# Optimization experiments

Hardware: AMD Instinct MI355X
Metric: run time of the kernel (lower is better)

The kernel has to match this reference:

```python
import jax, jax.numpy as jnp
import numpy as np

B, N, H = 32, 256, 1024
HEADS, NHID = 8, 128
NCLS = 7
BAND = 24
ALPHA = 0.2          # GAT leaky-relu slope
NEG = -9e15          # masked-attention fill, as in pyGAT


def setup_inputs() -> dict:
    key = jax.random.key(0)
    ks = jax.random.split(key, 16)
    def nrm(k, shp, s=0.02):
        return jax.random.normal(k, shp, dtype=jnp.float32) * s
    hidden_cls = jax.random.normal(ks[0], (B, N, H), dtype=jnp.float32)
    hidden_emo = jax.random.normal(ks[1], (B, N, H), dtype=jnp.float32)
    # causal band cliques, diagonal included (GAT uses clique - eye)
    t = jnp.arange(N)
    band = ((t[None, :] <= t[:, None]) & (t[None, :] > t[:, None] - BAND)).astype(jnp.float32)
    clique = jnp.broadcast_to(band, (B, N, N))
    labels = jax.random.randint(ks[2], (B, N), 0, NCLS)
    pooler_W = nrm(ks[3], (H, H)); pooler_b = jnp.zeros((H,), jnp.float32)
    gat_W = nrm(ks[4], (HEADS, H, NHID))
    gat_a1 = nrm(ks[5], (HEADS, NHID)); gat_a2 = nrm(ks[6], (HEADS, NHID))
    out_W = nrm(ks[7], (H, H))            # heads*nhid == H -> nclass=H
    out_a1 = nrm(ks[8], (H,)); out_a2 = nrm(ks[9], (H,))
    lin1_W = nrm(ks[10], (H, H)); lin1_b = jnp.zeros((H,), jnp.float32)
    lin0_W = nrm(ks[11], (2 * H, H)); lin0_b = jnp.zeros((H,), jnp.float32)
    cls_W = nrm(ks[12], (H, NCLS)); cls_b = jnp.zeros((NCLS,), jnp.float32)
    A = jax.random.uniform(ks[13], (NCLS, NCLS), dtype=jnp.float32) + 0.1
    hmm_A = A / A.sum(axis=1, keepdims=True)   # row-stochastic transition matrix
    return dict(hidden_cls=hidden_cls, hidden_emo=hidden_emo, clique=clique,
                labels=labels, pooler_W=pooler_W, pooler_b=pooler_b,
                gat_W=gat_W, gat_a1=gat_a1, gat_a2=gat_a2,
                out_W=out_W, out_a1=out_a1, out_a2=out_a2,
                lin1_W=lin1_W, lin1_b=lin1_b, lin0_W=lin0_W, lin0_b=lin0_b,
                cls_W=cls_W, cls_b=cls_b, hmm_A=hmm_A)


def _lrelu(x):
    return jnp.where(x > 0, x, ALPHA * x)


def reference(hidden_cls, hidden_emo, clique, labels, pooler_W, pooler_b,
              gat_W, gat_a1, gat_a2, out_W, out_a1, out_a2,
              lin1_W, lin1_b, lin0_W, lin0_b, cls_W, cls_b, hmm_A):
    # PoolerAll: dense + tanh on all token states (dropout = identity in eval)
    fea_cls = jnp.tanh(hidden_cls @ pooler_W + pooler_b)   # [B,N,H] (CLS per utt)
    fea_emo = jnp.tanh(hidden_emo @ pooler_W + pooler_b)   # [B,N,H] (mask tok per utt)

    eyeN = jnp.eye(N, dtype=clique.dtype)
    adjm = (clique - eyeN) > 0                             # [B,N,N] GAT adjacency

    def gat_one(x, am):                                    # x [N,H], am [N,N]
        Wh = jnp.einsum('nf,hfd->hnd', x, gat_W)           # [heads,N,nhid]
        e = _lrelu(jnp.einsum('hnd,hd->hn', Wh, gat_a1)[:, :, None]
                   + jnp.einsum('hnd,hd->hn', Wh, gat_a2)[:, None, :])
        att = jax.nn.softmax(jnp.where(am[None], e, NEG), axis=-1)
        h1 = jax.nn.elu(jnp.einsum('hnm,hmd->hnd', att, Wh))
        h1 = jnp.transpose(h1, (1, 0, 2)).reshape(N, HEADS * NHID)
        Wh2 = h1 @ out_W                                   # out attention layer (concat=False)
        e2 = _lrelu((Wh2 @ out_a1)[:, None] + (Wh2 @ out_a2)[None, :])
        h2 = jax.nn.softmax(jnp.where(am, e2, NEG), axis=-1) @ Wh2
        return jax.nn.elu(h2)                              # [N,H]

    gat_out = jax.vmap(gat_one)(fea_cls, adjm)             # [B,N,H]
    # row 0 replaced by (dropout of) fea_cls row 0, as in the original
    g = jnp.concatenate([fea_cls[:, :1], gat_out[:, 1:]], axis=1)
    g = jnp.concatenate([fea_cls, g @ lin1_W + lin1_b], axis=-1) @ lin0_W + lin0_b
    log_gat = jax.nn.softmax(g @ cls_W + cls_b, axis=-1)   # [B,N,NCLS] (probs)

    # HMM emission probs hmm_B(fea) = softmax(classifier(fea))
    Bprob = jax.nn.softmax(fea_emo @ cls_W + cls_b, axis=-1)  # [B,N,NCLS]
    P0 = jnp.full((NCLS,), 1.0 / NCLS, dtype=jnp.float32)
    AT = hmm_A.T

    def hmm_row(Bp, mrow):                                 # Bp [N,NCLS], mrow [N]
        def step(carry, xs):
            p, started = carry
            bt, m = xs
            p_init = P0 * bt; p_init = p_init / p_init.sum()
            p_tr = (AT @ p) * bt; p_tr = p_tr / p_tr.sum()
            p_new = jnp.where(started, p_tr, p_init)
            valid = m > 0.5
            return (jnp.where(valid, p_new, p), started | valid), None
        (p, _), _ = jax.lax.scan(step, (P0, jnp.asarray(False)), (Bp, mrow))
        return p                                           # final filtered posterior

    log_hmm = jax.vmap(lambda Bp, M: jax.vmap(lambda mr: hmm_row(Bp, mr))(M))(Bprob, clique)

    logits = jnp.log((log_gat + log_hmm) * 0.5).reshape(B * N, NCLS)
    lab = labels.reshape(B * N)
    mask = lab >= 0
    picked = jnp.take_along_axis(logits, jnp.where(mask, lab, 0)[:, None], axis=1)[:, 0]
    loss = -(jnp.where(mask, picked, 0.0).sum() / jnp.maximum(mask.sum(), 1).astype(jnp.float32))
    return loss, logits
```

## Files before the change

kernel.cpp:

```cpp
#include <hip/hip_runtime.h>
#include <hip/hip_bf16.h>
#include <math.h>

typedef __hip_bfloat16 bf16;
typedef __attribute__((ext_vector_type(8))) short short8;
typedef __attribute__((ext_vector_type(4))) float float4v;

static constexpr int Bb = 32, Nn = 256, Hh = 1024, HEADS = 8, NHID = 128, NCLS = 7, BAND = 24;
static constexpr int M = Bb * Nn;
static constexpr float ALPHA = 0.2f;
static constexpr long INEL = (long)M * Hh;

__device__ __forceinline__ float tof(bf16 x) { return __bfloat162float(x); }
__device__ __forceinline__ bf16 tob(float x) { return __float2bfloat16(x); }
__device__ __forceinline__ unsigned short f2bits(float x) {
    bf16 h = __float2bfloat16(x);
    return *(unsigned short*)&h;
}
__device__ __forceinline__ float bits2f(unsigned short u) {
    unsigned v = ((unsigned)u) << 16;
    float f;
    __builtin_memcpy(&f, &v, 4);
    return f;
}

__device__ __forceinline__ void gload16(const void* g, void* l) {
    __builtin_amdgcn_global_load_lds(
        (const __attribute__((address_space(1))) void*)g,
        (__attribute__((address_space(3))) void*)l, 16, 0, 0);
}

static constexpr long OFF_PWT  = 0;
static constexpr long OFF_PB   = 1048576;
static constexpr long OFF_WCT  = 1049600;
static constexpr long OFF_GA1  = 2098176;
static constexpr long OFF_GA2  = 2099200;
static constexpr long OFF_OWT  = 2100224;
static constexpr long OFF_OA1  = 3148800;
static constexpr long OFF_OA2  = 3149824;
static constexpr long OFF_CWT  = 6298624;
static constexpr long OFF_CB   = 6305792;
static constexpr long OFF_HA   = 6305799;
static constexpr long W_TOTAL  = 6305848;

__device__ __forceinline__ float ldany(const void* p, long i, int isb) {
    return isb ? tof(((const bf16*)p)[i]) : ((const float*)p)[i];
}

__device__ __forceinline__ int probe_dev(const void* pW, int t, int* sb) {
    int bad = 0;
    for (int i = t; i < 4096; i += 256) {
        float v = tof(((const bf16*)pW)[i]);
        if (!(fabsf(v) < 1e4f)) bad = 1;
    }
    sb[t] = bad; __syncthreads();
    for (int s = 128; s; s >>= 1) { if (t < s) sb[t] |= sb[t + s]; __syncthreads(); }
    int isb = sb[0] ? 0 : 1;
    __syncthreads();
    return isb;
}

__global__ __launch_bounds__(256) void prep1_k(
    const void* pW, const void* pb, const void* gW, const void* ga1,
    const void* ga2, const void* oW, const void* oa1, const void* oa2,
    const void* l0W, const void* cW, const void* cb, const void* hA,
    const void* in_emo, const void* in_cls,
    bf16* __restrict__ wc, int* __restrict__ flag,
    float* __restrict__ W1T, float* __restrict__ Gb,
    bf16* __restrict__ d0, bf16* __restrict__ d1) {
    __shared__ float SM[7168];
    const int bx = blockIdx.x;
    const int t = threadIdx.x;
    const int isb = probe_dev(pW, t, (int*)SM);

    if (bx == 0) {
        if (t == 0) *flag = isb;
        for (int i = t; i < 1024; i += 256) {
            wc[OFF_PB  + i] = tob(ldany(pb,  i, isb));
            wc[OFF_GA1 + i] = tob(ldany(ga1, i, isb));
            wc[OFF_GA2 + i] = tob(ldany(ga2, i, isb));
            wc[OFF_OA1 + i] = tob(ldany(oa1, i, isb));
            wc[OFF_OA2 + i] = tob(ldany(oa2, i, isb));
        }
        for (int i = t; i < 7168; i += 256) {
            int c = i >> 10, k = i & 1023;
            wc[OFF_CWT + i] = tob(ldany(cW, (long)k * 7 + c, isb));
        }
        if (t < NCLS) wc[OFF_CB + t] = tob(ldany(cb, t, isb));
        if (t < NCLS * NCLS) wc[OFF_HA + t] = tob(ldany(hA, t, isb));
        return;
    }
    if (bx < 1 + 2560) {
        int bi = bx - 1;
        int z = bi >> 8, rem = bi & 255;
        int bxx = rem & 15, byy = rem >> 4;
        float (*S)[65] = (float(*)[65])SM;
        const int tx = t & 63, ty0 = t >> 6;
        if (z < 2) {
            const void* src = z ? oW : pW;
            const long doff = z ? OFF_OWT : OFF_PWT;
            const int r0 = byy * 64, c0 = bxx * 64;
            #pragma unroll 4
            for (int it = 0; it < 16; ++it) {
                int ty = it * 4 + ty0;
                S[ty][tx] = ldany(src, (long)(r0 + ty) * 1024 + c0 + tx, isb);
            }
            __syncthreads();
            #pragma unroll 4
            for (int it = 0; it < 16; ++it) {
                int ty = it * 4 + ty0;
                wc[doff + (long)(c0 + ty) * 1024 + r0 + tx] = tob(S[tx][ty]);
            }
        } else {
            if (bxx >= 2) return;
            const int h = z - 2;
            const int r0 = byy * 64, c0 = bxx * 64;
            const long sbase = (long)h * 131072;
            #pragma unroll 4
            for (int it = 0; it < 16; ++it) {
                int ty = it * 4 + ty0;
                S[ty][tx] = ldany(gW, sbase + (long)(r0 + ty) * 128 + c0 + tx, isb);
            }
            __syncthreads();
            #pragma unroll 4
            for (int it = 0; it < 16; ++it) {
                int ty = it * 4 + ty0;
                wc[OFF_WCT + (long)(h * 128 + c0 + ty) * 1024 + r0 + tx] = tob(S[tx][ty]);
            }
        }
        return;
    }
    if (bx < 1 + 2560 + 256) {
        int bi = bx - 2561;
        float (*S)[NCLS] = (float(*)[NCLS])SM;
        for (int j = t; j < 1024; j += 256) {
            #pragma unroll
            for (int c = 0; c < NCLS; ++c) S[j][c] = ldany(cW, (long)j * 7 + c, isb);
        }
        __syncthreads();
        const int wave = t >> 6, lane = t & 63;
        #pragma unroll
        for (int r = 0; r < 2; ++r) {
            int k = bi * 8 + wave * 2 + r;
            float acc[NCLS];
            #pragma unroll
            for (int c = 0; c < NCLS; ++c) acc[c] = 0.f;
            #pragma unroll
            for (int q = 0; q < 16; ++q) {
                int j = lane * 16 + q;
                float x = ldany(l0W, (long)k * 1024 + j, isb);
                #pragma unroll
                for (int c = 0; c < NCLS; ++c) acc[c] += x * S[j][c];
            }
            #pragma unroll
            for (int c = 0; c < NCLS; ++c)
                #pragma unroll
                for (int off = 32; off; off >>= 1) acc[c] += __shfl_down(acc[c], off);
            if (lane == 0) {
                #pragma unroll
                for (int c = 0; c < NCLS; ++c) {
                    if (k < 1024) W1T[c * 1024 + k] = acc[c];
                    else          Gb[(k - 1024) * 7 + c] = acc[c];
                }
            }
        }
        return;
    }
    if (isb) return;
    long bi = bx - 2817;
    long i = (bi * 256 + t) * 8;
    const void* s; bf16* d; long off;
    if (i < INEL) { s = in_emo; d = d0; off = i; }
    else          { s = in_cls; d = d1; off = i - INEL; }
    const float* f = (const float*)s + off;
    unsigned short tmp[8];
    #pragma unroll
    for (int q = 0; q < 8; ++q) tmp[q] = f2bits(f[q]);
    *(int4*)(d + off) = *(int4*)tmp;
}

__global__ __launch_bounds__(256) void prep2_k(const int* __restrict__ flagp,
                                               const void* __restrict__ l1W,
                                               const void* __restrict__ l1b,
                                               const void* __restrict__ l0b,
                                               const void* __restrict__ cW,
                                               const void* __restrict__ cb,
                                               const float* __restrict__ Gb,
                                               float* __restrict__ W2T,
                                               float* __restrict__ cvec) {
    __shared__ float S[1024][NCLS];
    const int bx = blockIdx.x;
    const int t = threadIdx.x;
    const int isb = *flagp;
    if (bx < 128) {
        for (int j = t; j < 1024; j += 256) {
            #pragma unroll
            for (int c = 0; c < NCLS; ++c) S[j][c] = Gb[(long)j * 7 + c];
        }
        __syncthreads();
        const int wave = t >> 6, lane = t & 63;
        #pragma unroll
        for (int r = 0; r < 2; ++r) {
            int i = bx * 8 + wave * 2 + r;
            float acc[NCLS];
            #pragma unroll
            for (int c = 0; c < NCLS; ++c) acc[c] = 0.f;
            #pragma unroll
            for (int q = 0; q < 16; ++q) {
                int o = lane * 16 + q;
                float x = ldany(l1W, (long)i * 1024 + o, isb);
                #pragma unroll
                for (int c = 0; c < NCLS; ++c) acc[c] += x * S[o][c];
            }
            #pragma unroll
            for (int c = 0; c < NCLS; ++c)
                #pragma unroll
                for (int off = 32; off; off >>= 1) acc[c] += __shfl_down(acc[c], off);
            if (lane == 0) {
                #pragma unroll
                for (int c = 0; c < NCLS; ++c) W2T[c * 1024 + i] = acc[c];
            }
        }
        return;
    }
    if (t >= 64) return;
    int lane = t;
    float acc[NCLS];
    #pragma unroll
    for (int c = 0; c < NCLS; ++c) acc[c] = 0.f;
    for (int o = lane; o < 1024; o += 64) {
        float b1 = ldany(l1b, o, isb);
        float b0 = ldany(l0b, o, isb);
        #pragma unroll
        for (int c = 0; c < NCLS; ++c)
            acc[c] += b1 * Gb[o * 7 + c] + b0 * ldany(cW, (long)o * 7 + c, isb);
    }
    #pragma unroll
    for (int c = 0; c < NCLS; ++c)
        #pragma unroll
        for (int off = 32; off; off >>= 1) acc[c] += __shfl_down(acc[c], off);
    if (lane == 0) {
        #pragma unroll
        for (int c = 0; c < NCLS; ++c) cvec[c] = acc[c] + ldany(cb, c, isb);
    }
}

static constexpr int SLOT_US = 256 * 32;

template <int ACT, int DOTS>
__device__ __forceinline__ void gemm_pipe_core(
    const bf16* __restrict__ A, int strideA,
    const bf16* __restrict__ Bt, int strideB,
    const bf16* __restrict__ bias, bf16* __restrict__ Cout,
    int Nc, int K, int bm, int bn, unsigned short* lds,
    const bf16* __restrict__ oa1 = nullptr, const bf16* __restrict__ oa2 = nullptr,
    float* __restrict__ f1b = nullptr, float* __restrict__ f2b = nullptr) {
    const int tid = threadIdx.x;
    const int lane = tid & 63;
    const int wave = tid >> 6;
    const int wm = (wave >> 1) * 64, wn = (wave & 1) * 64;
    const int l15 = lane & 15, quad = lane >> 4;
    const int csw = ((lane & 3) ^ ((lane >> 2) & 3) ^ (lane >> 4)) * 8;
    const int sc8 = (quad ^ (l15 & 3) ^ (l15 >> 2)) * 8;

    long aoff[2], boff[2];
    #pragma unroll
    for (int o = 0; o < 2; ++o) {
        aoff[o] = (long)(bm + wave * 32 + o * 16 + (lane >> 2)) * strideA + csw;
        boff[o] = (long)(bn + wave * 32 + o * 16 + (lane >> 2)) * strideB + csw;
    }
    const int aDst = wave * 32 * 32;
    const int bDst = (128 + wave * 32) * 32;

    const int nt = K / 32;
    float4v acc[4][4];
    #pragma unroll
    for (int i = 0; i < 4; ++i)
        #pragma unroll
        for (int j = 0; j < 4; ++j) acc[i][j] = (float4v){0.f, 0.f, 0.f, 0.f};

    auto stage = [&](int ts, int slot) {
        unsigned short* buf = lds + slot * SLOT_US;
        int k = ts * 32;
        gload16(A + aoff[0] + k, buf + aDst);
        gload16(A + aoff[1] + k, buf + aDst + 512);
        gload16(Bt + boff[0] + k, buf + bDst);
        gload16(Bt + boff[1] + k, buf + bDst + 512);
    };
    auto frags = [&](int slot, short8* af, short8* bfr) {
        const unsigned short* bufc = lds + slot * SLOT_US;
        #pragma unroll
        for (int i = 0; i < 4; ++i)
            af[i] = *(const short8*)(bufc + (wm + i * 16 + l15) * 32 + sc8);
        #pragma unroll
        for (int j = 0; j < 4; ++j)
            bfr[j] = *(const short8*)(bufc + (128 + wn + j * 16 + l15) * 32 + sc8);
    };

    stage(0, 0); stage(1, 1); stage(2, 2);
    asm volatile("s_waitcnt vmcnt(8)" ::: "memory");
    __builtin_amdgcn_s_barrier();
    asm volatile("" ::: "memory");
    short8 afA[4], bfA[4], afB[4], bfB[4];
    frags(0, afA, bfA);
    int c0 = 0, c1 = 1, c2 = 2;

    for (int t = 0; t < nt; t += 2) {
        asm volatile("s_waitcnt lgkmcnt(0)" ::: "memory");
        if (t < nt - 2) asm volatile("s_waitcnt vmcnt(4)" ::: "memory");
        else            asm volatile("s_waitcnt vmcnt(0)" ::: "memory");
        __builtin_amdgcn_s_barrier();
        asm volatile("" ::: "memory");
        if (t + 3 < nt) stage(t + 3, c0);
        if (t + 1 < nt) frags(c1, afB, bfB);
        __builtin_amdgcn_s_setprio(1);
        #pragma unroll
        for (int i = 0; i < 4; ++i)
            #pragma unroll
            for (int j = 0; j < 4; ++j)
                acc[i][j] = __builtin_amdgcn_mfma_f32_16x16x32_bf16(afA[i], bfA[j], acc[i][j], 0, 0, 0);
        __builtin_amdgcn_s_setprio(0);
        asm volatile("" ::: "memory");
        asm volatile("s_waitcnt lgkmcnt(0)" ::: "memory");
        if (t + 1 < nt - 2) asm volatile("s_waitcnt vmcnt(4)" ::: "memory");
        else                asm volatile("s_waitcnt vmcnt(0)" ::: "memory");
        __builtin_amdgcn_s_barrier();
        asm volatile("" ::: "memory");
        if (t + 4 < nt) stage(t + 4, c1);
        if (t + 2 < nt) frags(c2, afA, bfA);
        __builtin_amdgcn_s_setprio(1);
        #pragma unroll
        for (int i = 0; i < 4; ++i)
            #pragma unroll
            for (int j = 0; j < 4; ++j)
                acc[i][j] = __builtin_amdgcn_mfma_f32_16x16x32_bf16(afB[i], bfB[j], acc[i][j], 0, 0, 0);
        __builtin_amdgcn_s_setprio(0);
        asm volatile("" ::: "memory");
        int n0 = c2, n1 = c0, n2 = c1;
        c0 = n0; c1 = n1; c2 = n2;
    }

    #pragma unroll
    for (int j = 0; j < 4; ++j) {
        int gn = bn + wn + j * 16 + l15;
        float bj = bias ? tof(bias[gn]) : 0.f;
        #pragma unroll
        for (int i = 0; i < 4; ++i) {
            #pragma unroll
            for (int r = 0; r < 4; ++r) {
                int gm = bm + wm + i * 16 + quad * 4 + r;
                float v = acc[i][j][r] + bj;
                if (ACT == 1) v = tanhf(v);
                Cout[(long)gm * Nc + gn] = tob(v);
            }
        }
    }
    if (DOTS) {
        float o1v[4], o2v[4];
        #pragma unroll
        for (int j = 0; j < 4; ++j) {
            int gn = bn + wn + j * 16 + l15;
            o1v[j] = tof(oa1[gn]); o2v[j] = tof(oa2[gn]);
        }
        #pragma unroll
        for (int i = 0; i < 4; ++i) {
            #pragma unroll
            for (int r = 0; r < 4; ++r) {
                int gm = bm + wm + i * 16 + quad * 4 + r;
                float p1 = 0.f, p2 = 0.f;
                #pragma unroll
                for (int j = 0; j < 4; ++j) {
                    float v = bits2f(f2bits(acc[i][j][r]));
                    p1 += v * o1v[j]; p2 += v * o2v[j];
                }
                #pragma unroll
                for (int m = 1; m < 16; m <<= 1) {
                    p1 += __shfl_xor(p1, m); p2 += __shfl_xor(p2, m);
                }
                if (l15 == 0) { atomicAdd(&f1b[gm], p1); atomicAdd(&f2b[gm], p2); }
            }
        }
    }
}

__global__ __launch_bounds__(256, 3) void gemmP_pipe_k(const int* __restrict__ flagp,
                                                       const bf16* __restrict__ rawE,
                                                       const bf16* __restrict__ rawC,
                                                       const bf16* __restrict__ A0,
                                                       const bf16* __restrict__ A1,
                                                       const bf16* __restrict__ Bt,
                                                       const bf16* __restrict__ bias,
                                                       bf16* __restrict__ C0,
                                                       bf16* __restrict__ C1) {
    __shared__ __align__(16) unsigned short lds[3 * SLOT_US];
    const int isb = *flagp;
    const bf16* A = blockIdx.z ? (isb ? rawC : A1) : (isb ? rawE : A0);
    bf16* C = blockIdx.z ? C1 : C0;
    gemm_pipe_core<1, 0>(A, Hh, Bt, Hh, bias, C, Hh, Hh,
                         blockIdx.x * 128, blockIdx.y * 128, lds);
}

__global__ __launch_bounds__(256, 3) void gemm_cls_k(const bf16* __restrict__ A,
                                                     const bf16* __restrict__ Bt,
                                                     bf16* __restrict__ Cout,
                                                     const bf16* __restrict__ X,
                                                     const bf16* __restrict__ Wt,
                                                     const bf16* __restrict__ cb,
                                                     float* __restrict__ Bout) {
    __shared__ __align__(16) unsigned short lds[3 * SLOT_US];
    const int bx = blockIdx.x;
    if (bx < 512) {
        gemm_pipe_core<0, 0>(A, Hh, Bt, Hh, (const bf16*)nullptr, Cout, Hh, Hh,
                             (bx & 63) * 128, (bx >> 6) * 128, lds);
        return;
    }
    const int t = threadIdx.x, wave = t >> 6, lane = t & 63;
    const int row = (bx - 512) * 4 + wave;
    float xv[16];
    {
        const bf16* x = X + (long)row * Hh + lane * 16;
        union { int4 v; unsigned short us[8]; } u0, u1;
        u0.v = *(const int4*)x; u1.v = *(const int4*)(x + 8);
        #pragma unroll
        for (int q = 0; q < 8; ++q) { xv[q] = bits2f(u0.us[q]); xv[q + 8] = bits2f(u1.us[q]); }
    }
    float acc[NCLS];
    #pragma unroll
    for (int cc = 0; cc < NCLS; ++cc) {
        const bf16* wr = Wt + (long)cc * Hh + lane * 16;
        union { int4 v; unsigned short us[8]; } w0, w1;
        w0.v = *(const int4*)wr; w1.v = *(const int4*)(wr + 8);
        float s = 0.f;
        #pragma unroll
        for (int q = 0; q < 8; ++q) {
            s += xv[q] * bits2f(w0.us[q]);
            s += xv[q + 8] * bits2f(w1.us[q]);
        }
        acc[cc] = s;
    }
    #pragma unroll
    for (int cc = 0; cc < NCLS; ++cc)
        #pragma unroll
        for (int off = 32; off; off >>= 1) acc[cc] += __shfl_down(acc[cc], off);
    if (lane == 0) {
        float mx = -1e30f;
        #pragma unroll
        for (int cc = 0; cc < NCLS; ++cc) { acc[cc] += tof(cb[cc]); mx = fmaxf(mx, acc[cc]); }
        float s = 0.f;
        #pragma unroll
        for (int cc = 0; cc < NCLS; ++cc) { acc[cc] = expf(acc[cc] - mx); s += acc[cc]; }
        float inv = 1.0f / s;
        #pragma unroll
        for (int cc = 0; cc < NCLS; ++cc) Bout[(long)row * NCLS + cc] = acc[cc] * inv;
    }
}

__global__ __launch_bounds__(256, 3) void gemm_f12_k(const bf16* __restrict__ A,
                                                     const bf16* __restrict__ Bt,
                                                     bf16* __restrict__ Cout,
                                                     const bf16* __restrict__ oa1,
                                                     const bf16* __restrict__ oa2,
                                                     float* __restrict__ f1b,
                                                     float* __restrict__ f2b) {
    __shared__ __align__(16) unsigned short lds[3 * SLOT_US];
    gemm_pipe_core<0, 1>(A, Hh, Bt, Hh, (const bf16*)nullptr, Cout, Hh, Hh,
                         blockIdx.x * 128, blockIdx.y * 128, lds, oa1, oa2, f1b, f2b);
}

__global__ __launch_bounds__(256) void att1f_k(const bf16* __restrict__ Wh,
                                               const bf16* __restrict__ ga1,
                                               const bf16* __restrict__ ga2,
                                               bf16* __restrict__ h1) {
    __shared__ unsigned short S[152][128];
    __shared__ float f1s[152], f2s[152];
    __shared__ float att[128][25];
    const int bx = blockIdx.x;
    const int t = threadIdx.x;
    const int wave = t >> 6, lane = t & 63;
    if (bx < 256) {
        int h = bx & 7, b = bx >> 3;
        float s0 = 0.f, s1 = 0.f;
        long base = (long)(b * 256) * 1024 + h * 128 + lane * 2;
        for (int m = wave * 64; m < wave * 64 + 64; ++m) {
            unsigned u = *(const unsigned*)(Wh + base + (long)m * 1024);
            s0 += bits2f((unsigned short)(u & 0xffff));
            s1 += bits2f((unsigned short)(u >> 16));
        }
        float* red = (float*)S;
        red[(wave * 64 + lane) * 2]     = s0;
        red[(wave * 64 + lane) * 2 + 1] = s1;
        __syncthreads();
        if (wave == 0) {
            s0 = red[lane * 2] + red[(64 + lane) * 2] + red[(128 + lane) * 2] + red[(192 + lane) * 2];
            s1 = red[lane * 2 + 1] + red[(64 + lane) * 2 + 1] + red[(128 + lane) * 2 + 1] + red[(192 + lane) * 2 + 1];
            s0 *= (1.0f / 256.0f); s1 *= (1.0f / 256.0f);
            s0 = s0 > 0.f ? s0 : expm1f(s0);
            s1 = s1 > 0.f ? s1 : expm1f(s1);
            unsigned out = (unsigned)f2bits(s0) | ((unsigned)f2bits(s1) << 16);
            *(unsigned*)(h1 + base) = out;
        }
        return;
    }
    const int bxm = bx - 256;
    const int b = bxm >> 4, h = (bxm >> 1) & 7, half = bxm & 1;
    const int nbase = half * 128;
    const int mstart = half ? (nbase - (BAND - 1)) : 0;
    const int mcount = half ? (256 - mstart) : 128;
    const int c = t & 15;

    float av1[8], av2[8];
    {
        union { int4 v; unsigned short us[8]; } u1, u2;
        u1.v = *(const int4*)(ga1 + h * 128 + c * 8);
        u2.v = *(const int4*)(ga2 + h * 128 + c * 8);
        #pragma unroll
        for (int qq = 0; qq < 8; ++qq) { av1[qq] = bits2f(u1.us[qq]); av2[qq] = bits2f(u2.us[qq]); }
    }

    const int iters = (mcount * 16 + 255) >> 8;
    for (int i = 0; i < iters; ++i) {
        int li = i * 256 + t;
        int mr = li >> 4;
        if (mr < mcount) {
            long ga = (long)(b * 256 + mstart + mr) * 1024 + h * 128 + c * 8;
            union { int4 v; unsigned short us[8]; } u;
            u.v = *(const int4*)(Wh + ga);
            float p1 = 0.f, p2 = 0.f;
            #pragma unroll
            for (int qq = 0; qq < 8; ++qq) {
                float f = bits2f(u.us[qq]);
                p1 += f * av1[qq]; p2 += f * av2[qq];
            }
            *(int4*)&S[mr][c * 8] = u.v;
            #pragma unroll
            for (int mask = 1; mask < 16; mask <<= 1) {
                p1 += __shfl_xor(p1, mask);
                p2 += __shfl_xor(p2, mask);
            }
            if (c == 0) { f1s[mr] = p1; f2s[mr] = p2; }
        }
    }
    __syncthreads();

    if (t < 128) {
        int n = nbase + t;
        if (n > 0) {
            int cnt = n < (BAND - 1) ? n : (BAND - 1);
            int m0 = n - cnt;
            float f1n = f1s[n - mstart];
            float e[BAND - 1];
            float mx = -1e30f;
            for (int i = 0; i < cnt; ++i) {
                float v = f1n + f2s[m0 + i - mstart];
                v = v > 0.f ? v : ALPHA * v;
                e[i] = v; mx = fmaxf(mx, v);
            }
            float ss = 0.f;
            for (int i = 0; i < cnt; ++i) { e[i] = __expf(e[i] - mx); ss += e[i]; }
            float inv = 1.0f / ss;
            for (int i = 0; i < cnt; ++i) att[t][i] = e[i] * inv;
        }
    }
    __syncthreads();

    for (int ln = wave; ln < 128; ln += 4) {
        int n = nbase + ln;
        if (n == 0) continue;
        int cnt = n < (BAND - 1) ? n : (BAND - 1);
        int mr0 = n - cnt - mstart;
        float s0 = 0.f, s1 = 0.f;
        for (int i = 0; i < cnt; ++i) {
            float a = att[ln][i];
            unsigned u = *(const unsigned*)&S[mr0 + i][lane * 2];
            s0 += a * bits2f((unsigned short)(u & 0xffff));
            s1 += a * bits2f((unsigned short)(u >> 16));
        }
        s0 = s0 > 0.f ? s0 : expm1f(s0);
        s1 = s1 > 0.f ? s1 : expm1f(s1);
        unsigned out = (unsigned)f2bits(s0) | ((unsigned)f2bits(s1) << 16);
        *(unsigned*)(h1 + (long)(b * 256 + n) * 1024 + h * 128 + lane * 2) = out;
    }
}

__global__ __launch_bounds__(256) void att2f_hmm_k(const bf16* __restrict__ Wh2,
                                                   const float* __restrict__ f1b,
                                                   const float* __restrict__ f2b,
                                                   bf16* __restrict__ g,
                                                   const float* __restrict__ Bprob,
                                                   const bf16* __restrict__ hmm_A,
                                                   float* __restrict__ lhmm) {
    __shared__ unsigned short S[152][128];
    __shared__ float att[128][25];
    __shared__ float AT[NCLS][NCLS];
    const int bx = blockIdx.x;
    const int t = threadIdx.x;
    if (bx >= 512) {
        if (t < NCLS * NCLS) {
            int i = t / NCLS, j = t % NCLS;
            AT[i][j] = tof(hmm_A[j * NCLS + i]);
        }
        __syncthreads();
        int idx = (bx - 512) * 256 + t;
        int n = idx & 255, b = idx >> 8;
        int t0 = n - (BAND - 1) > 0 ? n - (BAND - 1) : 0;
        const float* Bp = Bprob + (long)(b * 256) * NCLS;
        float p[NCLS];
        float s = 0.f;
        #pragma unroll
        for (int cc = 0; cc < NCLS; ++cc) { p[cc] = Bp[t0 * NCLS + cc]; s += p[cc]; }
        float inv = 1.0f / s;
        #pragma unroll
        for (int cc = 0; cc < NCLS; ++cc) p[cc] *= inv;
        for (int tt = t0 + 1; tt <= n; ++tt) {
            float q[NCLS]; float ss = 0.f;
            #pragma unroll
            for (int i = 0; i < NCLS; ++i) {
                float a = 0.f;
                #pragma unroll
                for (int j = 0; j < NCLS; ++j) a += AT[i][j] * p[j];
                a *= Bp[tt * NCLS + i];
                q[i] = a; ss += a;
            }
            float iv = 1.0f / ss;
            #pragma unroll
            for (int i = 0; i < NCLS; ++i) p[i] = q[i] * iv;
        }
        #pragma unroll
        for (int cc = 0; cc < NCLS; ++cc) lhmm[(long)idx * NCLS + cc] = p[cc];
        return;
    }
    const int b = bx >> 4, half = (bx >> 3) & 1, jt = bx & 7;
    const int nbase = half * 128;
    const int mstart = half ? (nbase - (BAND - 1)) : 0;
    const int mcount = half ? (256 - mstart) : 128;
    const int c = t & 15;

    const int iters = (mcount * 16 + 255) >> 8;
    for (int i = 0; i < iters; ++i) {
        int li = i * 256 + t;
        int mr = li >> 4;
        if (mr < mcount) {
            long ga = (long)(b * 256 + mstart + mr) * 1024 + jt * 128 + c * 8;
            *(int4*)&S[mr][c * 8] = *(const int4*)(Wh2 + ga);
        }
    }
    __syncthreads();

    if (t < 128) {
        int n = nbase + t;
        if (n > 0) {
            int cnt = n < (BAND - 1) ? n : (BAND - 1);
            int m0 = n - cnt;
            float f1n = f1b[b * 256 + n];
            float e[BAND - 1];
            float mx = -1e30f;
            for (int i = 0; i < cnt; ++i) {
                float v = f1n + f2b[b * 256 + m0 + i];
                v = v > 0.f ? v : ALPHA * v;
                e[i] = v; mx = fmaxf(mx, v);
            }
            float ss = 0.f;
            for (int i = 0; i < cnt; ++i) { e[i] = __expf(e[i] - mx); ss += e[i]; }
            float inv = 1.0f / ss;
            for (int i = 0; i < cnt; ++i) att[t][i] = e[i] * inv;
        }
    }
    __syncthreads();

    const int wave = t >> 6, lane = t & 63;
    for (int ln = wave; ln < 128; ln += 4) {
        int n = nbase + ln;
        if (n == 0) continue;
        int cnt = n < (BAND - 1) ? n : (BAND - 1);
        int mr0 = n - cnt - mstart;
        float s0 = 0.f, s1 = 0.f;
        for (int i = 0; i < cnt; ++i) {
            float a = att[ln][i];
            unsigned u = *(const unsigned*)&S[mr0 + i][lane * 2];
            s0 += a * bits2f((unsigned short)(u & 0xffff));
            s1 += a * bits2f((unsigned short)(u >> 16));
        }
        s0 = s0 > 0.f ? s0 : expm1f(s0);
        s1 = s1 > 0.f ? s1 : expm1f(s1);
        unsigned out = (unsigned)f2bits(s0) | ((unsigned)f2bits(s1) << 16);
        *(unsigned*)(g + (long)(b * 256 + n) * 1024 + jt * 128 + lane * 2) = out;
    }
}

__global__ __launch_bounds__(256) void lgf_k(const bf16* __restrict__ X,
                                             const bf16* __restrict__ Y,
                                             const float* __restrict__ W1T,
                                             const float* __restrict__ W2T,
                                             const float* __restrict__ cvec,
                                             const float* __restrict__ lhmm,
                                             const int* __restrict__ labels,
                                             void* __restrict__ out,
                                             float* __restrict__ blocksum,
                                             const int* __restrict__ flagp) {
    __shared__ float ps[4];
    const int t = threadIdx.x, wave = t >> 6, lane = t & 63;
    const int row = blockIdx.x * 4 + wave;
    const int isb = *flagp;
    const bf16* ybase = (row & 255) ? Y : X;
    float xv[16], yv[16];
    {
        const bf16* x = X + (long)row * 1024 + lane * 16;
        const bf16* y = ybase + (long)row * 1024 + lane * 16;
        union { int4 v; unsigned short us[8]; } u0, u1, v0, v1;
        u0.v = *(const int4*)x; u1.v = *(const int4*)(x + 8);
        v0.v = *(const int4*)y; v1.v = *(const int4*)(y + 8);
        #pragma unroll
        for (int q = 0; q < 8; ++q) {
            xv[q] = bits2f(u0.us[q]); xv[q + 8] = bits2f(u1.us[q]);
            yv[q] = bits2f(v0.us[q]); yv[q + 8] = bits2f(v1.us[q]);
        }
    }
    float acc[NCLS];
    #pragma unroll
    for (int cc = 0; cc < NCLS; ++cc) {
        const float4* w1 = (const float4*)(W1T + (long)cc * 1024 + lane * 16);
        const float4* w2 = (const float4*)(W2T + (long)cc * 1024 + lane * 16);
        float s = 0.f;
        #pragma unroll
        for (int h = 0; h < 4; ++h) {
            float4 a = w1[h], b = w2[h];
            s += xv[h * 4 + 0] * a.x + xv[h * 4 + 1] * a.y + xv[h * 4 + 2] * a.z + xv[h * 4 + 3] * a.w;
            s += yv[h * 4 + 0] * b.x + yv[h * 4 + 1] * b.y + yv[h * 4 + 2] * b.z + yv[h * 4 + 3] * b.w;
        }
        acc[cc] = s;
    }
    #pragma unroll
    for (int cc = 0; cc < NCLS; ++cc)
        #pragma unroll
        for (int off = 32; off; off >>= 1) acc[cc] += __shfl_down(acc[cc], off);
    if (lane == 0) {
        float mx = -1e30f;
        #pragma unroll
        for (int cc = 0; cc < NCLS; ++cc) { acc[cc] += cvec[cc]; mx = fmaxf(mx, acc[cc]); }
        float s = 0.f;
        #pragma unroll
        for (int cc = 0; cc < NCLS; ++cc) { acc[cc] = expf(acc[cc] - mx); s += acc[cc]; }
        float inv = 1.0f / s;
        int lab = labels[row];
        float picked = 0.f;
        #pragma unroll
        for (int cc = 0; cc < NCLS; ++cc) {
            float pg = acc[cc] * inv;
            float v = logf(0.5f * (pg + lhmm[(long)row * NCLS + cc]));
            long o = 1 + (long)row * NCLS + cc;
            if (isb) ((bf16*)out)[o] = tob(v);
            else     ((float*)out)[o] = v;
            if (cc == lab) picked = v;
        }
        ps[wave] = picked;
    }
    __syncthreads();
    if (t == 0) blocksum[blockIdx.x] = ps[0] + ps[1] + ps[2] + ps[3];
}

__global__ __launch_bounds__(256) void loss2_k(const float* __restrict__ blocksum,
                                               void* __restrict__ out,
                                               const int* __restrict__ flagp) {
    __shared__ float red[256];
    const int t = threadIdx.x;
    float s = 0.f;
    #pragma unroll
    for (int i = 0; i < 8; ++i) s += blocksum[t + i * 256];
    red[t] = s; __syncthreads();
    for (int st = 128; st; st >>= 1) {
        if (t < st) red[t] += red[t + st];
        __syncthreads();
    }
    if (t == 0) {
        float v = -red[0] / (float)(Bb * Nn);
        if (*flagp) ((bf16*)out)[0] = tob(v);
        else        ((float*)out)[0] = v;
    }
}

extern "C" void kernel_launch(void* const* d_in, const int* in_sizes, int n_in,
                              void* d_out, int out_size, void* d_ws, size_t ws_size,
                              hipStream_t stream) {
    const void* hidden_cls = d_in[0];
    const void* hidden_emo = d_in[1];
    const int* labels = (const int*)d_in[3];

    char* w = (char*)d_ws;
    bf16* C  = (bf16*)w;
    bf16* E  = C + INEL;
    bf16* Wb = E + INEL;
    bf16* H2 = Wb + INEL;
    bf16* wc = H2 + INEL;
    float* f1b      = (float*)(wc + W_TOTAL);
    float* f2b      = f1b + M;
    float* blocksum = f2b + M;
    int*   flag  = (int*)(blocksum + 2048);
    float* Bprob = (float*)(flag + 1);
    float* lhmm  = Bprob + (long)M * NCLS;
    float* W1f   = lhmm + (long)M * NCLS;
    float* W2f   = W1f + 7 * 1024;
    float* Gbf   = W2f + 7 * 1024;
    float* cvec  = Gbf + 1024 * 7;

    dim3 gblk(256);

    prep1_k<<<11009, gblk, 0, stream>>>(
        d_in[4], d_in[5], d_in[6], d_in[7], d_in[8], d_in[9], d_in[10], d_in[11],
        d_in[14], d_in[16], d_in[17], d_in[18], hidden_emo, hidden_cls,
        wc, flag, W1f, Gbf, Wb, H2);
    prep2_k<<<129, gblk, 0, stream>>>(flag, d_in[12], d_in[13], d_in[15],
                                      d_in[16], d_in[17], Gbf, W2f, cvec);
    gemmP_pipe_k<<<dim3(64, 8, 2), gblk, 0, stream>>>(
        flag, (const bf16*)hidden_emo, (const bf16*)hidden_cls, Wb, H2,
        wc + OFF_PWT, wc + OFF_PB, E, C);
    gemm_cls_k<<<512 + 2048, gblk, 0, stream>>>(C, wc + OFF_WCT, Wb,
                                                E, wc + OFF_CWT, wc + OFF_CB, Bprob);
    att1f_k<<<768, gblk, 0, stream>>>(Wb, wc + OFF_GA1, wc + OFF_GA2, E);
    (void)hipMemsetAsync(f1b, 0, (size_t)(2 * M) * 4, stream);
    gemm_f12_k<<<dim3(64, 8), gblk, 0, stream>>>(E, wc + OFF_OWT, Wb,
                                                 wc + OFF_OA1, wc + OFF_OA2, f1b, f2b);
    att2f_hmm_k<<<512 + 32, gblk, 0, stream>>>(Wb, f1b, f2b, E,
                                               Bprob, wc + OFF_HA, lhmm);
    lgf_k<<<2048, gblk, 0, stream>>>(C, E, W1f, W2f, cvec, lhmm, labels,
                                     d_out, blocksum, flag);
    loss2_k<<<1, gblk, 0, stream>>>(blocksum, d_out, flag);
}
```

Measured before the change: 461.7 us.

## Fuse all stages into one cooperative persistent kernel with grid syncs

Merges the prep, GEMM, attention, HMM and loss kernels into a single cooperative kernel. Blocks loop over the tasks of each phase, and grid-wide barriers separate the phases. This removes per-launch overhead and the separate memset, and the dtype probe now runs in every block instead of being passed through a flag. In exchange, the grid is capped at occupancy-limited size with a large shared-memory union, which may reduce GEMM occupancy and parallelism, and grid barriers add their own cost.

Result: slower. 888.4 us (+92.4%).

```diff
diff --git a/kernel.cpp b/kernel.cpp
--- a/kernel.cpp
+++ b/kernel.cpp
@@ -1,6 +1,9 @@
 #include <hip/hip_runtime.h>
 #include <hip/hip_bf16.h>
+#include <hip/hip_cooperative_groups.h>
 #include <math.h>
+
+namespace cg = cooperative_groups;
 
 typedef __hip_bfloat16 bf16;
 typedef __attribute__((ext_vector_type(8))) short short8;
@@ -43,9 +46,35 @@
 static constexpr long OFF_HA   = 6305799;
 static constexpr long W_TOTAL  = 6305848;
 
+static constexpr int SLOT_US = 256 * 32;
+
 __device__ __forceinline__ float ldany(const void* p, long i, int isb) {
     return isb ? tof(((const bf16*)p)[i]) : ((const float*)p)[i];
 }
+
+union ShU {
+    int sb[256];
+    unsigned short gemm[3 * SLOT_US];
+    float prep[7168];
+    struct { unsigned short S[152][128];
+             float f1s[152], f2s[152];
+             float att[128][25]; } a1;
+    struct { unsigned short S[152][128];
+             float att[128][25];
+             float AT[NCLS][NCLS]; } a2;
+    float ps[4];
+    float red[256];
+};
+
+struct MegaArgs {
+    const void *pW, *pb, *gW, *ga1, *ga2, *oW, *oa1, *oa2;
+    const void *l1W, *l1b, *l0W, *l0b, *cW, *cb, *hA;
+    const void *in_emo, *in_cls;
+    const int* labels;
+    bf16 *wc, *C, *E, *Wb, *H2;
+    float *f1b, *f2b, *blocksum, *Bprob, *lhmm, *W1T, *W2T, *Gb, *cvec;
+    void* out;
+};
 
 __device__ __forceinline__ int probe_dev(const void* pW, int t, int* sb) {
     int bad = 0;
@@ -60,44 +89,31 @@
     return isb;
 }
 
-__global__ __launch_bounds__(256) void prep1_k(
-    const void* pW, const void* pb, const void* gW, const void* ga1,
-    const void* ga2, const void* oW, const void* oa1, const void* oa2,
-    const void* l0W, const void* cW, const void* cb, const void* hA,
-    const void* in_emo, const void* in_cls,
-    bf16* __restrict__ wc, int* __restrict__ flag,
-    float* __restrict__ W1T, float* __restrict__ Gb,
-    bf16* __restrict__ d0, bf16* __restrict__ d1) {
-    __shared__ float SM[7168];
-    const int bx = blockIdx.x;
-    const int t = threadIdx.x;
-    const int isb = probe_dev(pW, t, (int*)SM);
-
-    if (bx == 0) {
-        if (t == 0) *flag = isb;
-        for (int i = t; i < 1024; i += 256) {
-            wc[OFF_PB  + i] = tob(ldany(pb,  i, isb));
-            wc[OFF_GA1 + i] = tob(ldany(ga1, i, isb));
-            wc[OFF_GA2 + i] = tob(ldany(ga2, i, isb));
-            wc[OFF_OA1 + i] = tob(ldany(oa1, i, isb));
-            wc[OFF_OA2 + i] = tob(ldany(oa2, i, isb));
-        }
-        for (int i = t; i < 7168; i += 256) {
-            int c = i >> 10, k = i & 1023;
-            wc[OFF_CWT + i] = tob(ldany(cW, (long)k * 7 + c, isb));
-        }
-        if (t < NCLS) wc[OFF_CB + t] = tob(ldany(cb, t, isb));
-        if (t < NCLS * NCLS) wc[OFF_HA + t] = tob(ldany(hA, t, isb));
-        return;
-    }
-    if (bx < 1 + 2560) {
-        int bi = bx - 1;
-        int z = bi >> 8, rem = bi & 255;
+__device__ void smalls_task(const MegaArgs& a, int t, int isb) {
+    bf16* wc = a.wc;
+    for (int i = t; i < 1024; i += 256) {
+        wc[OFF_PB  + i] = tob(ldany(a.pb,  i, isb));
+        wc[OFF_GA1 + i] = tob(ldany(a.ga1, i, isb));
+        wc[OFF_GA2 + i] = tob(ldany(a.ga2, i, isb));
+        wc[OFF_OA1 + i] = tob(ldany(a.oa1, i, isb));
+        wc[OFF_OA2 + i] = tob(ldany(a.oa2, i, isb));
+    }
+    for (int i = t; i < 7168; i += 256) {
+        int c = i >> 10, k = i & 1023;
+        wc[OFF_CWT + i] = tob(ldany(a.cW, (long)k * 7 + c, isb));
+    }
+    if (t < NCLS) wc[OFF_CB + t] = tob(ldany(a.cb, t, isb));
+    if (t < NCLS * NCLS) wc[OFF_HA + t] = tob(ldany(a.hA, t, isb));
+}
+
+__device__ void prep_mid_task(int v, const MegaArgs& a, int t, int isb, ShU* sh) {
+    if (v < 2560) {
+        int z = v >> 8, rem = v & 255;
         int bxx = rem & 15, byy = rem >> 4;
-        float (*S)[65] = (float(*)[65])SM;
+        float (*S)[65] = (float(*)[65])sh->prep;
         const int tx = t & 63, ty0 = t >> 6;
         if (z < 2) {
-            const void* src = z ? oW : pW;
+            const void* src = z ? a.oW : a.pW;
             const long doff = z ? OFF_OWT : OFF_PWT;
             const int r0 = byy * 64, c0 = bxx * 64;
             #pragma unroll 4
@@ -109,7 +125,7 @@
             #pragma unroll 4
             for (int it = 0; it < 16; ++it) {
                 int ty = it * 4 + ty0;
-                wc[doff + (long)(c0 + ty) * 1024 + r0 + tx] = tob(S[tx][ty]);
+                a.wc[doff + (long)(c0 + ty) * 1024 + r0 + tx] = tob(S[tx][ty]);
             }
         } else {
             if (bxx >= 2) return;
@@ -119,121 +135,96 @@
             #pragma unroll 4
             for (int it = 0; it < 16; ++it) {
                 int ty = it * 4 + ty0;
-                S[ty][tx] = ldany(gW, sbase + (long)(r0 + ty) * 128 + c0 + tx, isb);
+                S[ty][tx] = ldany(a.gW, sbase + (long)(r0 + ty) * 128 + c0 + tx, isb);
             }
             __syncthreads();
             #pragma unroll 4
             for (int it = 0; it < 16; ++it) {
                 int ty = it * 4 + ty0;
-                wc[OFF_WCT + (long)(h * 128 + c0 + ty) * 1024 + r0 + tx] = tob(S[tx][ty]);
+                a.wc[OFF_WCT + (long)(h * 128 + c0 + ty) * 1024 + r0 + tx] = tob(S[tx][ty]);
             }
         }
         return;
     }
-    if (bx < 1 + 2560 + 256) {
-        int bi = bx - 2561;
-        float (*S)[NCLS] = (float(*)[NCLS])SM;
-        for (int j = t; j < 1024; j += 256) {
-            #pragma unroll
-            for (int c = 0; c < NCLS; ++c) S[j][c] = ldany(cW, (long)j * 7 + c, isb);
-        }
-        __syncthreads();
-        const int wave = t >> 6, lane = t & 63;
-        #pragma unroll
-        for (int r = 0; r < 2; ++r) {
-            int k = bi * 8 + wave * 2 + r;
-            float acc[NCLS];
-            #pragma unroll
-            for (int c = 0; c < NCLS; ++c) acc[c] = 0.f;
-            #pragma unroll
-            for (int q = 0; q < 16; ++q) {
-                int j = lane * 16 + q;
-                float x = ldany(l0W, (long)k * 1024 + j, isb);
-                #pragma unroll
-                for (int c = 0; c < NCLS; ++c) acc[c] += x * S[j][c];
-            }
-            #pragma unroll
-            for (int c = 0; c < NCLS; ++c)
-                #pragma unroll
-                for (int off = 32; off; off >>= 1) acc[c] += __shfl_down(acc[c], off);
-            if (lane == 0) {
-                #pragma unroll
-                for (int c = 0; c < NCLS; ++c) {
-                    if (k < 1024) W1T[c * 1024 + k] = acc[c];
-                    else          Gb[(k - 1024) * 7 + c] = acc[c];
-                }
-            }
-        }
-        return;
-    }
-    if (isb) return;
-    long bi = bx - 2817;
-    long i = (bi * 256 + t) * 8;
-    const void* s; bf16* d; long off;
-    if (i < INEL) { s = in_emo; d = d0; off = i; }
-    else          { s = in_cls; d = d1; off = i - INEL; }
-    const float* f = (const float*)s + off;
-    unsigned short tmp[8];
-    #pragma unroll
-    for (int q = 0; q < 8; ++q) tmp[q] = f2bits(f[q]);
-    *(int4*)(d + off) = *(int4*)tmp;
-}
-
-__global__ __launch_bounds__(256) void prep2_k(const int* __restrict__ flagp,
-                                               const void* __restrict__ l1W,
-                                               const void* __restrict__ l1b,
-                                               const void* __restrict__ l0b,
-                                               const void* __restrict__ cW,
-                                               const void* __restrict__ cb,
-                                               const float* __restrict__ Gb,
-                                               float* __restrict__ W2T,
-                                               float* __restrict__ cvec) {
-    __shared__ float S[1024][NCLS];
-    const int bx = blockIdx.x;
-    const int t = threadIdx.x;
-    const int isb = *flagp;
-    if (bx < 128) {
-        for (int j = t; j < 1024; j += 256) {
-            #pragma unroll
-            for (int c = 0; c < NCLS; ++c) S[j][c] = Gb[(long)j * 7 + c];
-        }
-        __syncthreads();
-        const int wave = t >> 6, lane = t & 63;
-        #pragma unroll
-        for (int r = 0; r < 2; ++r) {
-            int i = bx * 8 + wave * 2 + r;
-            float acc[NCLS];
-            #pragma unroll
-            for (int c = 0; c < NCLS; ++c) acc[c] = 0.f;
-            #pragma unroll
-            for (int q = 0; q < 16; ++q) {
-                int o = lane * 16 + q;
-                float x = ldany(l1W, (long)i * 1024 + o, isb);
-                #pragma unroll
-                for (int c = 0; c < NCLS; ++c) acc[c] += x * S[o][c];
-            }
-            #pragma unroll
-            for (int c = 0; c < NCLS; ++c)
-                #pragma unroll
-                for (int off = 32; off; off >>= 1) acc[c] += __shfl_down(acc[c], off);
-            if (lane == 0) {
-                #pragma unroll
-                for (int c = 0; c < NCLS; ++c) W2T[c * 1024 + i] = acc[c];
-            }
-        }
-        return;
-    }
+    int bi = v - 2560;
+    float (*S)[NCLS] = (float(*)[NCLS])sh->prep;
+    for (int j = t; j < 1024; j += 256) {
+        #pragma unroll
+        for (int c = 0; c < NCLS; ++c) S[j][c] = ldany(a.cW, (long)j * 7 + c, isb);
+    }
+    __syncthreads();
+    const int wave = t >> 6, lane = t & 63;
+    #pragma unroll
+    for (int r = 0; r < 2; ++r) {
+        int k = bi * 8 + wave * 2 + r;
+        float acc[NCLS];
+        #pragma unroll
+        for (int c = 0; c < NCLS; ++c) acc[c] = 0.f;
+        #pragma unroll
+        for (int q = 0; q < 16; ++q) {
+            int j = lane * 16 + q;
+            float x = ldany(a.l0W, (long)k * 1024 + j, isb);
+            #pragma unroll
+            for (int c = 0; c < NCLS; ++c) acc[c] += x * S[j][c];
+        }
+        #pragma unroll
+        for (int c = 0; c < NCLS; ++c)
+            #pragma unroll
+            for (int off = 32; off; off >>= 1) acc[c] += __shfl_down(acc[c], off);
+        if (lane == 0) {
+            #pragma unroll
+            for (int c = 0; c < NCLS; ++c) {
+                if (k < 1024) a.W1T[c * 1024 + k] = acc[c];
+                else          a.Gb[(k - 1024) * 7 + c] = acc[c];
+            }
+        }
+    }
+}
+
+__device__ void w2_task(int bi, const MegaArgs& a, int t, int isb, ShU* sh) {
+    float (*S)[NCLS] = (float(*)[NCLS])sh->prep;
+    for (int j = t; j < 1024; j += 256) {
+        #pragma unroll
+        for (int c = 0; c < NCLS; ++c) S[j][c] = a.Gb[(long)j * 7 + c];
+    }
+    __syncthreads();
+    const int wave = t >> 6, lane = t & 63;
+    #pragma unroll
+    for (int r = 0; r < 2; ++r) {
+        int i = bi * 8 + wave * 2 + r;
+        float acc[NCLS];
+        #pragma unroll
+        for (int c = 0; c < NCLS; ++c) acc[c] = 0.f;
+        #pragma unroll
+        for (int q = 0; q < 16; ++q) {
+            int o = lane * 16 + q;
+            float x = ldany(a.l1W, (long)i * 1024 + o, isb);
+            #pragma unroll
+            for (int c = 0; c < NCLS; ++c) acc[c] += x * S[o][c];
+        }
+        #pragma unroll
+        for (int c = 0; c < NCLS; ++c)
+            #pragma unroll
+            for (int off = 32; off; off >>= 1) acc[c] += __shfl_down(acc[c], off);
+        if (lane == 0) {
+            #pragma unroll
+            for (int c = 0; c < NCLS; ++c) a.W2T[c * 1024 + i] = acc[c];
+        }
+    }
+}
+
+__device__ void cvec_task(const MegaArgs& a, int t, int isb) {
     if (t >= 64) return;
     int lane = t;
     float acc[NCLS];
     #pragma unroll
     for (int c = 0; c < NCLS; ++c) acc[c] = 0.f;
     for (int o = lane; o < 1024; o += 64) {
-        float b1 = ldany(l1b, o, isb);
-        float b0 = ldany(l0b, o, isb);
+        float b1 = ldany(a.l1b, o, isb);
+        float b0 = ldany(a.l0b, o, isb);
         #pragma unroll
         for (int c = 0; c < NCLS; ++c)
-            acc[c] += b1 * Gb[o * 7 + c] + b0 * ldany(cW, (long)o * 7 + c, isb);
+            acc[c] += b1 * a.Gb[o * 7 + c] + b0 * ldany(a.cW, (long)o * 7 + c, isb);
     }
     #pragma unroll
     for (int c = 0; c < NCLS; ++c)
@@ -241,11 +232,9 @@
         for (int off = 32; off; off >>= 1) acc[c] += __shfl_down(acc[c], off);
     if (lane == 0) {
         #pragma unroll
-        for (int c = 0; c < NCLS; ++c) cvec[c] = acc[c] + ldany(cb, c, isb);
-    }
-}
-
-static constexpr int SLOT_US = 256 * 32;
+        for (int c = 0; c < NCLS; ++c) a.cvec[c] = acc[c] + ldany(a.cb, c, isb);
+    }
+}
 
 template <int ACT, int DOTS>
 __device__ __forceinline__ void gemm_pipe_core(
@@ -383,39 +372,10 @@
     }
 }
 
-__global__ __launch_bounds__(256, 3) void gemmP_pipe_k(const int* __restrict__ flagp,
-                                                       const bf16* __restrict__ rawE,
-                                                       const bf16* __restrict__ rawC,
-                                                       const bf16* __restrict__ A0,
-                                                       const bf16* __restrict__ A1,
-                                                       const bf16* __restrict__ Bt,
-                                                       const bf16* __restrict__ bias,
-                                                       bf16* __restrict__ C0,
-                                                       bf16* __restrict__ C1) {
-    __shared__ __align__(16) unsigned short lds[3 * SLOT_US];
-    const int isb = *flagp;
-    const bf16* A = blockIdx.z ? (isb ? rawC : A1) : (isb ? rawE : A0);
-    bf16* C = blockIdx.z ? C1 : C0;
-    gemm_pipe_core<1, 0>(A, Hh, Bt, Hh, bias, C, Hh, Hh,
-                         blockIdx.x * 128, blockIdx.y * 128, lds);
-}
-
-__global__ __launch_bounds__(256, 3) void gemm_cls_k(const bf16* __restrict__ A,
-                                                     const bf16* __restrict__ Bt,
-                                                     bf16* __restrict__ Cout,
-                                                     const bf16* __restrict__ X,
-                                                     const bf16* __restrict__ Wt,
-                                                     const bf16* __restrict__ cb,
-                                                     float* __restrict__ Bout) {
-    __shared__ __align__(16) unsigned short lds[3 * SLOT_US];
-    const int bx = blockIdx.x;
-    if (bx < 512) {
-        gemm_pipe_core<0, 0>(A, Hh, Bt, Hh, (const bf16*)nullptr, Cout, Hh, Hh,
-                             (bx & 63) * 128, (bx >> 6) * 128, lds);
-        return;
-    }
-    const int t = threadIdx.x, wave = t >> 6, lane = t & 63;
-    const int row = (bx - 512) * 4 + wave;
+__device__ void cls7_task(int vt, const bf16* X, const bf16* Wt, const bf16* cb,
+                          float* Bout, int t) {
+    const int wave = t >> 6, lane = t & 63;
+    const int row = vt * 4 + wave;
     float xv[16];
     {
         const bf16* x = X + (long)row * Hh + lane * 16;
@@ -455,30 +415,11 @@
     }
 }
 
-__global__ __launch_bounds__(256, 3) void gemm_f12_k(const bf16* __restrict__ A,
-                                                     const bf16* __restrict__ Bt,
-                                                     bf16* __restrict__ Cout,
-                                                     const bf16* __restrict__ oa1,
-                                                     const bf16* __restrict__ oa2,
-                                                     float* __restrict__ f1b,
-                                                     float* __restrict__ f2b) {
-    __shared__ __align__(16) unsigned short lds[3 * SLOT_US];
-    gemm_pipe_core<0, 1>(A, Hh, Bt, Hh, (const bf16*)nullptr, Cout, Hh, Hh,
-                         blockIdx.x * 128, blockIdx.y * 128, lds, oa1, oa2, f1b, f2b);
-}
-
-__global__ __launch_bounds__(256) void att1f_k(const bf16* __restrict__ Wh,
-                                               const bf16* __restrict__ ga1,
-                                               const bf16* __restrict__ ga2,
-                                               bf16* __restrict__ h1) {
-    __shared__ unsigned short S[152][128];
-    __shared__ float f1s[152], f2s[152];
-    __shared__ float att[128][25];
-    const int bx = blockIdx.x;
-    const int t = threadIdx.x;
+__device__ void att1_task(int v, const bf16* Wh, const bf16* ga1, const bf16* ga2,
+                          bf16* h1, int t, ShU* sh) {
     const int wave = t >> 6, lane = t & 63;
-    if (bx < 256) {
-        int h = bx & 7, b = bx >> 3;
+    if (v < 256) {
+        int h = v & 7, b = v >> 3;
         float s0 = 0.f, s1 = 0.f;
         long base = (long)(b * 256) * 1024 + h * 128 + lane * 2;
         for (int m = wave * 64; m < wave * 64 + 64; ++m) {
@@ -486,7 +427,7 @@
             s0 += bits2f((unsigned short)(u & 0xffff));
             s1 += bits2f((unsigned short)(u >> 16));
         }
-        float* red = (float*)S;
+        float* red = (float*)sh;
         red[(wave * 64 + lane) * 2]     = s0;
         red[(wave * 64 + lane) * 2 + 1] = s1;
         __syncthreads();
@@ -501,7 +442,7 @@
         }
         return;
     }
-    const int bxm = bx - 256;
+    const int bxm = v - 256;
     const int b = bxm >> 4, h = (bxm >> 1) & 7, half = bxm & 1;
     const int nbase = half * 128;
     const int mstart = half ? (nbase - (BAND - 1)) : 0;
@@ -510,9 +451,9 @@
 
     float av1[8], av2[8];
     {
-        union { int4 v; unsigned short us[8]; } u1, u2;
-        u1.v = *(const int4*)(ga1 + h * 128 + c * 8);
-        u2.v = *(const int4*)(ga2 + h * 128 + c * 8);
+        union { int4 v4; unsigned short us[8]; } u1, u2;
+        u1.v4 = *(const int4*)(ga1 + h * 128 + c * 8);
+        u2.v4 = *(const int4*)(ga2 + h * 128 + c * 8);
         #pragma unroll
         for (int qq = 0; qq < 8; ++qq) { av1[qq] = bits2f(u1.us[qq]); av2[qq] = bits2f(u2.us[qq]); }
     }
@@ -523,21 +464,21 @@
         int mr = li >> 4;
         if (mr < mcount) {
             long ga = (long)(b * 256 + mstart + mr) * 1024 + h * 128 + c * 8;
-            union { int4 v; unsigned short us[8]; } u;
-            u.v = *(const int4*)(Wh + ga);
+            union { int4 v4; unsigned short us[8]; } u;
+            u.v4 = *(const int4*)(Wh + ga);
             float p1 = 0.f, p2 = 0.f;
             #pragma unroll
             for (int qq = 0; qq < 8; ++qq) {
                 float f = bits2f(u.us[qq]);
                 p1 += f * av1[qq]; p2 += f * av2[qq];
             }
-            *(int4*)&S[mr][c * 8] = u.v;
+            *(int4*)&sh->a1.S[mr][c * 8] = u.v4;
             #pragma unroll
             for (int mask = 1; mask < 16; mask <<= 1) {
                 p1 += __shfl_xor(p1, mask);
                 p2 += __shfl_xor(p2, mask);
             }
-            if (c == 0) { f1s[mr] = p1; f2s[mr] = p2; }
+            if (c == 0) { sh->a1.f1s[mr] = p1; sh->a1.f2s[mr] = p2; }
         }
     }
     __syncthreads();
@@ -547,18 +488,18 @@
         if (n > 0) {
             int cnt = n < (BAND - 1) ? n : (BAND - 1);
             int m0 = n - cnt;
-            float f1n = f1s[n - mstart];
+            float f1n = sh->a1.f1s[n - mstart];
             float e[BAND - 1];
             float mx = -1e30f;
             for (int i = 0; i < cnt; ++i) {
-                float v = f1n + f2s[m0 + i - mstart];
-                v = v > 0.f ? v : ALPHA * v;
-                e[i] = v; mx = fmaxf(mx, v);
+                float vv = f1n + sh->a1.f2s[m0 + i - mstart];
+                vv = vv > 0.f ? vv : ALPHA * vv;
+                e[i] = vv; mx = fmaxf(mx, vv);
             }
             float ss = 0.f;
             for (int i = 0; i < cnt; ++i) { e[i] = __expf(e[i] - mx); ss += e[i]; }
             float inv = 1.0f / ss;
-            for (int i = 0; i < cnt; ++i) att[t][i] = e[i] * inv;
+            for (int i = 0; i < cnt; ++i) sh->a1.att[t][i] = e[i] * inv;
         }
     }
     __syncthreads();
@@ -570,10 +511,10 @@
         int mr0 = n - cnt - mstart;
         float s0 = 0.f, s1 = 0.f;
         for (int i = 0; i < cnt; ++i) {
-            float a = att[ln][i];
-            unsigned u = *(const unsigned*)&S[mr0 + i][lane * 2];
-            s0 += a * bits2f((unsigned short)(u & 0xffff));
-            s1 += a * bits2f((unsigned short)(u >> 16));
+            float aa = sh->a1.att[ln][i];
+            unsigned u = *(const unsigned*)&sh->a1.S[mr0 + i][lane * 2];
+            s0 += aa * bits2f((unsigned short)(u & 0xffff));
+            s1 += aa * bits2f((unsigned short)(u >> 16));
         }
         s0 = s0 > 0.f ? s0 : expm1f(s0);
         s1 = s1 > 0.f ? s1 : expm1f(s1);
@@ -582,28 +523,18 @@
     }
 }
 
-__global__ __launch_bounds__(256) void att2f_hmm_k(const bf16* __restrict__ Wh2,
-                                                   const float* __restrict__ f1b,
-                                                   const float* __restrict__ f2b,
-                                                   bf16* __restrict__ g,
-                                                   const float* __restrict__ Bprob,
-                                                   const bf16* __restrict__ hmm_A,
-                                                   float* __restrict__ lhmm) {
-    __shared__ unsigned short S[152][128];
-    __shared__ float att[128][25];
-    __shared__ float AT[NCLS][NCLS];
-    const int bx = blockIdx.x;
-    const int t = threadIdx.x;
-    if (bx >= 512) {
+__device__ void att2_hmm_task(int v, const MegaArgs& a, int t, ShU* sh) {
+    const int wave = t >> 6, lane = t & 63;
+    if (v >= 512) {
         if (t < NCLS * NCLS) {
             int i = t / NCLS, j = t % NCLS;
-            AT[i][j] = tof(hmm_A[j * NCLS + i]);
+            sh->a2.AT[i][j] = tof((a.wc + OFF_HA)[j * NCLS + i]);
         }
         __syncthreads();
-        int idx = (bx - 512) * 256 + t;
+        int idx = (v - 512) * 256 + t;
         int n = idx & 255, b = idx >> 8;
         int t0 = n - (BAND - 1) > 0 ? n - (BAND - 1) : 0;
-        const float* Bp = Bprob + (long)(b * 256) * NCLS;
+        const float* Bp = a.Bprob + (long)(b * 256) * NCLS;
         float p[NCLS];
         float s = 0.f;
         #pragma unroll
@@ -615,25 +546,26 @@
             float q[NCLS]; float ss = 0.f;
             #pragma unroll
             for (int i = 0; i < NCLS; ++i) {
-                float a = 0.f;
+                float av = 0.f;
                 #pragma unroll
-                for (int j = 0; j < NCLS; ++j) a += AT[i][j] * p[j];
-                a *= Bp[tt * NCLS + i];
-                q[i] = a; ss += a;
+                for (int j = 0; j < NCLS; ++j) av += sh->a2.AT[i][j] * p[j];
+                av *= Bp[tt * NCLS + i];
+                q[i] = av; ss += av;
             }
             float iv = 1.0f / ss;
             #pragma unroll
             for (int i = 0; i < NCLS; ++i) p[i] = q[i] * iv;
         }
         #pragma unroll
-        for (int cc = 0; cc < NCLS; ++cc) lhmm[(long)idx * NCLS + cc] = p[cc];
+        for (int cc = 0; cc < NCLS; ++cc) a.lhmm[(long)idx * NCLS + cc] = p[cc];
         return;
     }
-    const int b = bx >> 4, half = (bx >> 3) & 1, jt = bx & 7;
+    const int b = v >> 4, half = (v >> 3) & 1, jt = v & 7;
     const int nbase = half * 128;
     const int mstart = half ? (nbase - (BAND - 1)) : 0;
     const int mcount = half ? (256 - mstart) : 128;
     const int c = t & 15;
+    const bf16* Wh2 = a.Wb;
 
     const int iters = (mcount * 16 + 255) >> 8;
     for (int i = 0; i < iters; ++i) {
@@ -641,7 +573,7 @@
         int mr = li >> 4;
         if (mr < mcount) {
             long ga = (long)(b * 256 + mstart + mr) * 1024 + jt * 128 + c * 8;
-            *(int4*)&S[mr][c * 8] = *(const int4*)(Wh2 + ga);
+            *(int4*)&sh->a2.S[mr][c * 8] = *(const int4*)(Wh2 + ga);
         }
     }
     __syncthreads();
@@ -651,23 +583,22 @@
         if (n > 0) {
             int cnt = n < (BAND - 1) ? n : (BAND - 1);
             int m0 = n - cnt;
-            float f1n = f1b[b * 256 + n];
+            float f1n = a.f1b[b * 256 + n];
             float e[BAND - 1];
             float mx = -1e30f;
             for (int i = 0; i < cnt; ++i) {
-                float v = f1n + f2b[b * 256 + m0 + i];
-                v = v > 0.f ? v : ALPHA * v;
-                e[i] = v; mx = fmaxf(mx, v);
+                float vv = f1n + a.f2b[b * 256 + m0 + i];
+                vv = vv > 0.f ? vv : ALPHA * vv;
+                e[i] = vv; mx = fmaxf(mx, vv);
             }
             float ss = 0.f;
             for (int i = 0; i < cnt; ++i) { e[i] = __expf(e[i] - mx); ss += e[i]; }
             float inv = 1.0f / ss;
-            for (int i = 0; i < cnt; ++i) att[t][i] = e[i] * inv;
+            for (int i = 0; i < cnt; ++i) sh->a2.att[t][i] = e[i] * inv;
         }
     }
     __syncthreads();
 
-    const int wave = t >> 6, lane = t & 63;
     for (int ln = wave; ln < 128; ln += 4) {
         int n = nbase + ln;
         if (n == 0) continue;
@@ -675,40 +606,30 @@
         int mr0 = n - cnt - mstart;
         float s0 = 0.f, s1 = 0.f;
         for (int i = 0; i < cnt; ++i) {
-            float a = att[ln][i];
-            unsigned u = *(const unsigned*)&S[mr0 + i][lane * 2];
-            s0 += a * bits2f((unsigned short)(u & 0xffff));
-            s1 += a * bits2f((unsigned short)(u >> 16));
+            float aa = sh->a2.att[ln][i];
+            unsigned u = *(const unsigned*)&sh->a2.S[mr0 + i][lane * 2];
+            s0 += aa * bits2f((unsigned short)(u & 0xffff));
+            s1 += aa * bits2f((unsigned short)(u >> 16));
         }
         s0 = s0 > 0.f ? s0 : expm1f(s0);
         s1 = s1 > 0.f ? s1 : expm1f(s1);
         unsigned out = (unsigned)f2bits(s0) | ((unsigned)f2bits(s1) << 16);
-        *(unsigned*)(g + (long)(b * 256 + n) * 1024 + jt * 128 + lane * 2) = out;
-    }
-}
-
-__global__ __launch_bounds__(256) void lgf_k(const bf16* __restrict__ X,
-                                             const bf16* __restrict__ Y,
-                                             const float* __restrict__ W1T,
-                                             const float* __restrict__ W2T,
-                                             const float* __restrict__ cvec,
-                                             const float* __restrict__ lhmm,
-                                             const int* __restrict__ labels,
-                                             void* __restrict__ out,
-                                             float* __restrict__ blocksum,
-                                             const int* __restrict__ flagp) {
-    __shared__ float ps[4];
-    const int t = threadIdx.x, wave = t >> 6, lane = t & 63;
-    const int row = blockIdx.x * 4 + wave;
-    const int isb = *flagp;
-    const bf16* ybase = (row & 255) ? Y : X;
+        *(unsigned*)(a.E + (long)(b * 256 + n) * 1024 + jt * 128 + lane * 2) = out;
+    }
+}
+
+__device__ void lgf_task(int v, const MegaArgs& a, int t, int isb, ShU* sh) {
+    const int wave = t >> 6, lane = t & 63;
+    const int row = v * 4 + wave;
+    const bf16* X = a.C;
+    const bf16* ybase = (row & 255) ? a.E : a.C;
     float xv[16], yv[16];
     {
         const bf16* x = X + (long)row * 1024 + lane * 16;
         const bf16* y = ybase + (long)row * 1024 + lane * 16;
-        union { int4 v; unsigned short us[8]; } u0, u1, v0, v1;
-        u0.v = *(const int4*)x; u1.v = *(const int4*)(x + 8);
-        v0.v = *(const int4*)y; v1.v = *(const int4*)(y + 8);
+        union { int4 v4; unsigned short us[8]; } u0, u1, v0, v1;
+        u0.v4 = *(const int4*)x; u1.v4 = *(const int4*)(x + 8);
+        v0.v4 = *(const int4*)y; v1.v4 = *(const int4*)(y + 8);
         #pragma unroll
         for (int q = 0; q < 8; ++q) {
             xv[q] = bits2f(u0.us[q]); xv[q + 8] = bits2f(u1.us[q]);
@@ -718,14 +639,14 @@
     float acc[NCLS];
     #pragma unroll
     for (int cc = 0; cc < NCLS; ++cc) {
-        const float4* w1 = (const float4*)(W1T + (long)cc * 1024 + lane * 16);
-        const float4* w2 = (const float4*)(W2T + (long)cc * 1024 + lane * 16);
+        const float4* w1 = (const float4*)(a.W1T + (long)cc * 1024 + lane * 16);
+        const float4* w2 = (const float4*)(a.W2T + (long)cc * 1024 + lane * 16);
         float s = 0.f;
         #pragma unroll
         for (int h = 0; h < 4; ++h) {
-            float4 a = w1[h], b = w2[h];
-            s += xv[h * 4 + 0] * a.x + xv[h * 4 + 1] * a.y + xv[h * 4 + 2] * a.z + xv[h * 4 + 3] * a.w;
-            s += yv[h * 4 + 0] * b.x + yv[h * 4 + 1] * b.y + yv[h * 4 + 2] * b.z + yv[h * 4 + 3] * b.w;
+            float4 aa = w1[h], bb = w2[h];
+            s += xv[h * 4 + 0] * aa.x + xv[h * 4 + 1] * aa.y + xv[h * 4 + 2] * aa.z + xv[h * 4 + 3] * aa.w;
+            s += yv[h * 4 + 0] * bb.x + yv[h * 4 + 1] * bb.y + yv[h * 4 + 2] * bb.z + yv[h * 4 + 3] * bb.w;
         }
         acc[cc] = s;
     }
@@ -736,55 +657,124 @@
     if (lane == 0) {
         float mx = -1e30f;
         #pragma unroll
-        for (int cc = 0; cc < NCLS; ++cc) { acc[cc] += cvec[cc]; mx = fmaxf(mx, acc[cc]); }
+        for (int cc = 0; cc < NCLS; ++cc) { acc[cc] += a.cvec[cc]; mx = fmaxf(mx, acc[cc]); }
         float s = 0.f;
         #pragma unroll
         for (int cc = 0; cc < NCLS; ++cc) { acc[cc] = expf(acc[cc] - mx); s += acc[cc]; }
         float inv = 1.0f / s;
-        int lab = labels[row];
+        int lab = a.labels[row];
         float picked = 0.f;
         #pragma unroll
         for (int cc = 0; cc < NCLS; ++cc) {
             float pg = acc[cc] * inv;
-            float v = logf(0.5f * (pg + lhmm[(long)row * NCLS + cc]));
+            float vv = logf(0.5f * (pg + a.lhmm[(long)row * NCLS + cc]));
             long o = 1 + (long)row * NCLS + cc;
-            if (isb) ((bf16*)out)[o] = tob(v);
-            else     ((float*)out)[o] = v;
-            if (cc == lab) picked = v;
-        }
-        ps[wave] = picked;
+            if (isb) ((bf16*)a.out)[o] = tob(vv);
+            else     ((float*)a.out)[o] = vv;
+            if (cc == lab) picked = vv;
+        }
+        sh->ps[wave] = picked;
     }
     __syncthreads();
-    if (t == 0) blocksum[blockIdx.x] = ps[0] + ps[1] + ps[2] + ps[3];
-}
-
-__global__ __launch_bounds__(256) void loss2_k(const float* __restrict__ blocksum,
-                                               void* __restrict__ out,
-                                               const int* __restrict__ flagp) {
-    __shared__ float red[256];
-    const int t = threadIdx.x;
-    float s = 0.f;
-    #pragma unroll
-    for (int i = 0; i < 8; ++i) s += blocksum[t + i * 256];
-    red[t] = s; __syncthreads();
-    for (int st = 128; st; st >>= 1) {
-        if (t < st) red[t] += red[t + st];
+    if (t == 0) a.blocksum[v] = sh->ps[0] + sh->ps[1] + sh->ps[2] + sh->ps[3];
+}
+
+__global__ void __launch_bounds__(256, 2) mega_k(MegaArgs a) {
+    __shared__ ShU sh;
+    cg::grid_group grid = cg::this_grid();
+    const int bx = blockIdx.x, t = threadIdx.x, G = gridDim.x;
+    const int isb = probe_dev(a.pW, t, sh.sb);
+
+    if (bx == 0) smalls_task(a, t, isb);
+    for (int v = bx; v < 2816; v += G) { prep_mid_task(v, a, t, isb, &sh); __syncthreads(); }
+    if (!isb) {
+        const long total = 2 * INEL / 8;
+        for (long idx = (long)bx * 256 + t; idx < total; idx += (long)G * 256) {
+            long i = idx * 8;
+            const void* s; bf16* d; long off;
+            if (i < INEL) { s = a.in_emo; d = a.Wb; off = i; }
+            else          { s = a.in_cls; d = a.H2; off = i - INEL; }
+            const float* f = (const float*)s + off;
+            unsigned short tmp[8];
+            #pragma unroll
+            for (int q = 0; q < 8; ++q) tmp[q] = f2bits(f[q]);
+            *(int4*)(d + off) = *(int4*)tmp;
+        }
+    }
+    for (long i = (long)bx * 256 + t; i < 2 * M; i += (long)G * 256) a.f1b[i] = 0.f;
+    grid.sync();
+
+    for (int v = bx; v < 1024; v += G) {
+        int z = v >> 9, rem = v & 511;
+        const bf16* A = z ? (isb ? (const bf16*)a.in_cls : a.H2)
+                          : (isb ? (const bf16*)a.in_emo : a.Wb);
+        bf16* Co = z ? a.C : a.E;
+        gemm_pipe_core<1, 0>(A, Hh, a.wc + OFF_PWT, Hh, a.wc + OFF_PB, Co, Hh, Hh,
+                             (rem & 63) * 128, (rem >> 6) * 128, sh.gemm);
         __syncthreads();
     }
-    if (t == 0) {
-        float v = -red[0] / (float)(Bb * Nn);
-        if (*flagp) ((bf16*)out)[0] = tob(v);
-        else        ((float*)out)[0] = v;
+    grid.sync();
+
+    for (int v = bx; v < 2689; v += G) {
+        if (v < 512)
+            gemm_pipe_core<0, 0>(a.C, Hh, a.wc + OFF_WCT, Hh, (const bf16*)nullptr,
+                                 a.Wb, Hh, Hh, (v & 63) * 128, (v >> 6) * 128, sh.gemm);
+        else if (v < 2560)
+            cls7_task(v - 512, a.E, a.wc + OFF_CWT, a.wc + OFF_CB, a.Bprob, t);
+        else if (v < 2688)
+            w2_task(v - 2560, a, t, isb, &sh);
+        else
+            cvec_task(a, t, isb);
+        __syncthreads();
+    }
+    grid.sync();
+
+    for (int v = bx; v < 768; v += G) {
+        att1_task(v, a.Wb, a.wc + OFF_GA1, a.wc + OFF_GA2, a.E, t, &sh);
+        __syncthreads();
+    }
+    grid.sync();
+
+    for (int v = bx; v < 512; v += G) {
+        gemm_pipe_core<0, 1>(a.E, Hh, a.wc + OFF_OWT, Hh, (const bf16*)nullptr,
+                             a.Wb, Hh, Hh, (v & 63) * 128, (v >> 6) * 128, sh.gemm,
+                             a.wc + OFF_OA1, a.wc + OFF_OA2, a.f1b, a.f2b);
+        __syncthreads();
+    }
+    grid.sync();
+
+    for (int v = bx; v < 544; v += G) {
+        att2_hmm_task(v, a, t, &sh);
+        __syncthreads();
+    }
+    grid.sync();
+
+    for (int v = bx; v < 2048; v += G) {
+        lgf_task(v, a, t, isb, &sh);
+        __syncthreads();
+    }
+    grid.sync();
+
+    if (bx == 0) {
+        float s = 0.f;
+        #pragma unroll
+        for (int i = 0; i < 8; ++i) s += a.blocksum[t + i * 256];
+        sh.red[t] = s; __syncthreads();
+        for (int st = 128; st; st >>= 1) {
+            if (t < st) sh.red[t] += sh.red[t + st];
+            __syncthreads();
+        }
+        if (t == 0) {
+            float v = -sh.red[0] / (float)(Bb * Nn);
+            if (isb) ((bf16*)a.out)[0] = tob(v);
+            else     ((float*)a.out)[0] = v;
+        }
     }
 }
 
 extern "C" void kernel_launch(void* const* d_in, const int* in_sizes, int n_in,
                               void* d_out, int out_size, void* d_ws, size_t ws_size,
                               hipStream_t stream) {
-    const void* hidden_cls = d_in[0];
-    const void* hidden_emo = d_in[1];
-    const int* labels = (const int*)d_in[3];
-
     char* w = (char*)d_ws;
     bf16* C  = (bf16*)w;
     bf16* E  = C + INEL;
@@ -794,34 +784,32 @@
     float* f1b      = (float*)(wc + W_TOTAL);
     float* f2b      = f1b + M;
     float* blocksum = f2b + M;
-    int*   flag  = (int*)(blocksum + 2048);
-    float* Bprob = (float*)(flag + 1);
+    float* Bprob = blocksum + 2048;
     float* lhmm  = Bprob + (long)M * NCLS;
     float* W1f   = lhmm + (long)M * NCLS;
     float* W2f   = W1f + 7 * 1024;
     float* Gbf   = W2f + 7 * 1024;
     float* cvec  = Gbf + 1024 * 7;
 
-    dim3 gblk(256);
-
-    prep1_k<<<11009, gblk, 0, stream>>>(
-        d_in[4], d_in[5], d_in[6], d_in[7], d_in[8], d_in[9], d_in[10], d_in[11],
-        d_in[14], d_in[16], d_in[17], d_in[18], hidden_emo, hidden_cls,
-        wc, flag, W1f, Gbf, Wb, H2);
-    prep2_k<<<129, gblk, 0, stream>>>(flag, d_in[12], d_in[13], d_in[15],
-                                      d_in[16], d_in[17], Gbf, W2f, cvec);
-    gemmP_pipe_k<<<dim3(64, 8, 2), gblk, 0, stream>>>(
-        flag, (const bf16*)hidden_emo, (const bf16*)hidden_cls, Wb, H2,
-        wc + OFF_PWT, wc + OFF_PB, E, C);
-    gemm_cls_k<<<512 + 2048, gblk, 0, stream>>>(C, wc + OFF_WCT, Wb,
-                                                E, wc + OFF_CWT, wc + OFF_CB, Bprob);
-    att1f_k<<<768, gblk, 0, stream>>>(Wb, wc + OFF_GA1, wc + OFF_GA2, E);
-    (void)hipMemsetAsync(f1b, 0, (size_t)(2 * M) * 4, stream);
-    gemm_f12_k<<<dim3(64, 8), gblk, 0, stream>>>(E, wc + OFF_OWT, Wb,
-                                                 wc + OFF_OA1, wc + OFF_OA2, f1b, f2b);
-    att2f_hmm_k<<<512 + 32, gblk, 0, stream>>>(Wb, f1b, f2b, E,
-                                               Bprob, wc + OFF_HA, lhmm);
-    lgf_k<<<2048, gblk, 0, stream>>>(C, E, W1f, W2f, cvec, lhmm, labels,
-                                     d_out, blocksum, flag);
-    loss2_k<<<1, gblk, 0, stream>>>(blocksum, d_out, flag);
-}
+    MegaArgs a;
+    a.pW = d_in[4];  a.pb = d_in[5];  a.gW = d_in[6];  a.ga1 = d_in[7];
+    a.ga2 = d_in[8]; a.oW = d_in[9];  a.oa1 = d_in[10]; a.oa2 = d_in[11];
+    a.l1W = d_in[12]; a.l1b = d_in[13]; a.l0W = d_in[14]; a.l0b = d_in[15];
+    a.cW = d_in[16]; a.cb = d_in[17]; a.hA = d_in[18];
+    a.in_emo = d_in[1]; a.in_cls = d_in[0];
+    a.labels = (const int*)d_in[3];
+    a.wc = wc; a.C = C; a.E = E; a.Wb = Wb; a.H2 = H2;
+    a.f1b = f1b; a.f2b = f2b; a.blocksum = blocksum; a.Bprob = Bprob;
+    a.lhmm = lhmm; a.W1T = W1f; a.W2T = W2f; a.Gb = Gbf; a.cvec = cvec;
+    a.out = d_out;
+
+    int maxB = 0;
+    if (hipOccupancyMaxActiveBlocksPerMultiprocessor(&maxB, mega_k, 256, 0)
+        != hipSuccess || maxB < 1) maxB = 1;
+    int gridB = maxB * 256;
+    if (gridB > 512) gridB = 512;
+
+    void* kargs[1] = { &a };
+    (void)hipLaunchCooperativeKernel((const void*)mega_k, dim3(gridB), dim3(256),
+                                     kargs, 0, stream);
+}
```
